# Kernel optimization log

Measured on AMD Instinct MI355X. Metric: run time of the kernel, lower is better.

Reference implementation:

```python
import jax, jax.numpy as jnp
import numpy as np

B, N, F, U, FE, T, E = 2, 50000, 256, 256, 128, 3, 131072


def setup_inputs() -> dict:
    key = jax.random.key(0)
    ks = jax.random.split(key, 7)
    features = jax.random.normal(ks[0], (B, N, F), dtype=jnp.float32)
    edge_idx = jax.random.randint(ks[1], (T, E), 0, B * N, dtype=jnp.int32)  # flattened (b*N+n)
    edge_feats = jax.random.normal(ks[2], (T, E, FE), dtype=jnp.float32)
    W_gate = jax.random.normal(ks[3], (F, U), dtype=jnp.float32) * (1.0 / np.sqrt(F))
    W_gate_e = jax.random.normal(ks[4], (T, FE, U), dtype=jnp.float32) * (1.0 / np.sqrt(FE))
    W_dense = jax.random.normal(ks[5], (T, FE, U), dtype=jnp.float32) * (1.0 / np.sqrt(FE))
    b_dense = jax.random.normal(ks[6], (T, U), dtype=jnp.float32) * 0.01
    return {"features": features, "edge_idx": edge_idx, "edge_feats": edge_feats,
            "W_gate": W_gate, "W_gate_e": W_gate_e, "W_dense": W_dense, "b_dense": b_dense}


def reference(features, edge_idx, edge_feats, W_gate, W_gate_e, W_dense, b_dense):
    b, n, f = features.shape
    u = W_gate.shape[1]
    # shared gate Dense (no bias) applied to all node features; flattened over (B,N)
    src_gated = features.reshape(b * n, f) @ W_gate                      # [B*N, U]
    # per-edge-type gate/value transforms, vectorized over edge types
    gate_e = jnp.einsum('tef,tfu->teu', edge_feats, W_gate_e)            # [T, E, U]
    val_e = jnp.einsum('tef,tfu->teu', edge_feats, W_dense) + b_dense[:, None, :]
    gate = jax.nn.sigmoid(src_gated[edge_idx] + gate_e)                  # gather node gate per edge
    msgs = val_e * gate                                                  # [T, E, U]
    out = jnp.zeros((b * n, u), features.dtype)
    out = out.at[edge_idx.reshape(-1)].add(msgs.reshape(-1, u))          # scatter-add over all edge types
    return out.reshape(b, n, u)
```

## Files before the change

### kernel.cpp

```cpp
#include <hip/hip_runtime.h>
#include <math.h>

#define M1 100000
#define FF 256
#define UU 256
#define FED 128
#define TT 3
#define EE 131072
#define EPB 32
#define TPT 8
#define EPA 32
#define SCAN_B 98

typedef __attribute__((ext_vector_type(8))) short short8;
typedef __attribute__((ext_vector_type(4))) short short4v;
typedef __attribute__((ext_vector_type(4))) float f32x4;

static __device__ __forceinline__ ushort f2bf(float x) {
    union { float f; uint u; } c; c.f = x;
    const uint u = c.u;
    return (ushort)((u + 0x7FFFu + ((u >> 16) & 1u)) >> 16);
}
static __device__ __forceinline__ float bf2f(ushort h) {
    union { uint u; float f; } c; c.u = ((uint)h) << 16;
    return c.f;
}

__global__ __launch_bounds__(256) void k_prep(const float* __restrict__ Wg,
                                              const float* __restrict__ Wge,
                                              const float* __restrict__ Wde,
                                              short* __restrict__ WtG,
                                              short* __restrict__ WtGe,
                                              short* __restrict__ WtDe) {
    const int idx = blockIdx.x * 256 + threadIdx.x;
    if (idx < 65536) {
        const int n = idx >> 8, k = idx & 255;
        WtG[n * 256 + k] = (short)f2bf(Wg[k * 256 + n]);
    } else {
        int j = idx - 65536;
        const float* src = Wge;
        short* dst = WtGe;
        if (j >= 98304) { j -= 98304; src = Wde; dst = WtDe; }
        const int t = j >> 15, rem = j & 32767;
        const int n = rem >> 7, k = rem & 127;
        dst[t * 32768 + n * 128 + k] = (short)f2bf(src[t * 32768 + k * 256 + n]);
    }
}

__global__ __launch_bounds__(256) void k1_srcgate(const float* __restrict__ feats,
                                                  const short* __restrict__ WtG,
                                                  ushort* __restrict__ sg) {
    __shared__ char As[32 * 512];
    const int tid = threadIdx.x, lane = tid & 63, wid = tid >> 6;
    const int r0 = blockIdx.x * 32;

    const float* src = feats + (size_t)r0 * FF;
#pragma unroll
    for (int j = 0; j < 4; ++j) {
        const int chunk = j * 256 + tid;
        const int row = chunk >> 5, kc = chunk & 31;
        const float4 f0 = *(const float4*)(src + row * FF + kc * 8);
        const float4 f1 = *(const float4*)(src + row * FF + kc * 8 + 4);
        short8 v;
        v[0]=(short)f2bf(f0.x); v[1]=(short)f2bf(f0.y); v[2]=(short)f2bf(f0.z); v[3]=(short)f2bf(f0.w);
        v[4]=(short)f2bf(f1.x); v[5]=(short)f2bf(f1.y); v[6]=(short)f2bf(f1.z); v[7]=(short)f2bf(f1.w);
        int byte = row * 512 + kc * 16;
        byte ^= (row & 7) << 4;
        *(short8*)(As + byte) = v;
    }
    __syncthreads();

    const int nb = wid * 64;
    f32x4 acc[2][4];
#pragma unroll
    for (int m = 0; m < 2; ++m)
#pragma unroll
        for (int n = 0; n < 4; ++n) acc[m][n] = (f32x4){0.f, 0.f, 0.f, 0.f};

    for (int ks = 0; ks < 8; ++ks) {
        short8 a[2];
#pragma unroll
        for (int m = 0; m < 2; ++m) {
            const int row = m * 16 + (lane & 15);
            int byte = row * 512 + ks * 64 + (lane >> 4) * 16;
            byte ^= (row & 7) << 4;
            a[m] = *(const short8*)(As + byte);
        }
#pragma unroll
        for (int n = 0; n < 4; ++n) {
            const int col = nb + n * 16 + (lane & 15);
            const short8 b = *(const short8*)(WtG + col * 256 + ks * 32 + (lane >> 4) * 8);
#pragma unroll
            for (int m = 0; m < 2; ++m)
                acc[m][n] = __builtin_amdgcn_mfma_f32_16x16x32_bf16(a[m], b, acc[m][n], 0, 0, 0);
        }
    }
#pragma unroll
    for (int m = 0; m < 2; ++m)
#pragma unroll
        for (int n = 0; n < 4; ++n) {
            const int col = nb + n * 16 + (lane & 15);
#pragma unroll
            for (int r = 0; r < 4; ++r) {
                const int row = m * 16 + (lane >> 4) * 4 + r;
                sg[(size_t)(r0 + row) * UU + col] = f2bf(acc[m][n][r]);
            }
        }
}

__global__ __launch_bounds__(256) void k_hist(const int* __restrict__ eidx,
                                              int* __restrict__ cnt) {
    const int idx = blockIdx.x * 256 + threadIdx.x;
    atomicAdd(&cnt[(idx >> 17) * M1 + eidx[idx]], 1);
}

__global__ __launch_bounds__(1024) void k_scan1(int* __restrict__ cnt,
                                                int* __restrict__ part) {
    const int t = blockIdx.x / SCAN_B, b = blockIdx.x % SCAN_B;
    const int i = b * 1024 + threadIdx.x;
    __shared__ int s[1024];
    const int v = (i < M1) ? cnt[t * M1 + i] : 0;
    s[threadIdx.x] = v;
    __syncthreads();
    for (int off = 1; off < 1024; off <<= 1) {
        const int x = (threadIdx.x >= off) ? s[threadIdx.x - off] : 0;
        __syncthreads();
        s[threadIdx.x] += x;
        __syncthreads();
    }
    if (i < M1) cnt[t * M1 + i] = s[threadIdx.x] - v;
    if (threadIdx.x == 1023) part[blockIdx.x] = s[1023];
}

__global__ void k_scan2(int* __restrict__ part) {
    const int t = threadIdx.x;
    if (t < TT) {
        int run = 0;
        for (int b = 0; b < SCAN_B; ++b) {
            const int p = part[t * SCAN_B + b];
            part[t * SCAN_B + b] = run;
            run += p;
        }
    }
}

__global__ __launch_bounds__(1024) void k_scan3(int* __restrict__ cnt,
                                                const int* __restrict__ part) {
    const int t = blockIdx.x / SCAN_B, b = blockIdx.x % SCAN_B;
    const int i = b * 1024 + threadIdx.x;
    if (i < M1) cnt[t * M1 + i] += part[blockIdx.x];
}

__global__ __launch_bounds__(256) void k_scatter(const int* __restrict__ eidx,
                                                 int* __restrict__ cur,
                                                 int* __restrict__ sorted,
                                                 int* __restrict__ snode) {
    const int idx = blockIdx.x * 256 + threadIdx.x;
    const int t = idx >> 17;
    const int v = eidx[idx];
    const int slot = atomicAdd(&cur[t * M1 + v], 1);
    sorted[t * EE + slot] = idx & (EE - 1);
    snode[t * EE + slot]  = v;
}

__global__ __launch_bounds__(1024, 4) void k2_msgs(const float* __restrict__ efeat,
                                                   const short* __restrict__ WtGe,
                                                   const short* __restrict__ WtDe,
                                                   const float* __restrict__ bd,
                                                   const ushort* __restrict__ sg,
                                                   const int* __restrict__ sorted,
                                                   const int* __restrict__ snode,
                                                   ushort* __restrict__ msgs) {
    __shared__ char As[EPB * 256];
    __shared__ ushort sgl[EPB][264];
    const int tid = threadIdx.x, lane = tid & 63, wid = tid >> 6;
    const int t = blockIdx.y;
    const int tile0 = blockIdx.x * TPT;

    const int col = wid * 16 + (lane & 15);
    const int ksl = (lane >> 4) * 8;
    const short* Bg = WtGe + t * 32768;
    const short* Bd = WtDe + t * 32768;
    short8 wg[4], wv[4];
#pragma unroll
    for (int ks = 0; ks < 4; ++ks) {
        wg[ks] = *(const short8*)(Bg + col * 128 + ks * 32 + ksl);
        wv[ks] = *(const short8*)(Bd + col * 128 + ks * 32 + ksl);
    }
    const float bias = bd[t * UU + col];

    const int erow = tid >> 5, ekc = tid & 31;

    float4 pf_e;
    uint4  pf_g;
    {
        const int base = t * EE + tile0 * EPB;
        const int se = sorted[base + erow];
        pf_e = *(const float4*)(efeat + ((size_t)t * EE + se) * FED + ekc * 4);
        const int nd = snode[base + erow];
        pf_g = *(const uint4*)((const uint*)(sg + (size_t)nd * UU) + ekc * 4);
    }

    for (int it = 0; it < TPT; ++it) {
        const int e0 = (tile0 + it) * EPB;

        {
            short4v v;
            v[0] = (short)f2bf(pf_e.x); v[1] = (short)f2bf(pf_e.y);
            v[2] = (short)f2bf(pf_e.z); v[3] = (short)f2bf(pf_e.w);
            int byte = erow * 256 + ekc * 8;
            byte ^= (erow & 7) << 4;
            *(short4v*)(As + byte) = v;
            *(uint4*)&sgl[erow][ekc * 8] = pf_g;
        }
        __syncthreads();

        if (it + 1 < TPT) {
            const int base = t * EE + (tile0 + it + 1) * EPB;
            const int se = sorted[base + erow];
            pf_e = *(const float4*)(efeat + ((size_t)t * EE + se) * FED + ekc * 4);
            const int nd = snode[base + erow];
            pf_g = *(const uint4*)((const uint*)(sg + (size_t)nd * UU) + ekc * 4);
        }

        f32x4 accg[2], accv[2];
#pragma unroll
        for (int m = 0; m < 2; ++m) {
            accg[m] = (f32x4){0.f, 0.f, 0.f, 0.f};
            accv[m] = (f32x4){bias, bias, bias, bias};
        }
#pragma unroll
        for (int ks = 0; ks < 4; ++ks) {
#pragma unroll
            for (int m = 0; m < 2; ++m) {
                const int row = m * 16 + (lane & 15);
                int byte = row * 256 + ks * 64 + (lane >> 4) * 16;
                byte ^= (row & 7) << 4;
                const short8 a = *(const short8*)(As + byte);
                accg[m] = __builtin_amdgcn_mfma_f32_16x16x32_bf16(a, wg[ks], accg[m], 0, 0, 0);
                accv[m] = __builtin_amdgcn_mfma_f32_16x16x32_bf16(a, wv[ks], accv[m], 0, 0, 0);
            }
        }

#pragma unroll
        for (int m = 0; m < 2; ++m) {
            const int ebase = m * 16 + (lane >> 4) * 4;
#pragma unroll
            for (int r = 0; r < 4; ++r) {
                const float sgv = bf2f(sgl[ebase + r][col]);
                const float e = __expf(-(sgv + accg[m][r]));
                const float g = __builtin_amdgcn_rcpf(1.f + e);
                const float msg = accv[m][r] * g;
                msgs[((size_t)t * EE + e0 + ebase + r) * UU + col] = f2bf(msg);
            }
        }
        __syncthreads();
    }
}

__global__ __launch_bounds__(256, 8) void k3_reduce(const int* __restrict__ cnt,
                                                    const ushort* __restrict__ msgs,
                                                    float* __restrict__ out) {
    const int tid = threadIdx.x, lane = tid & 63, w = tid >> 6;
    const int v = blockIdx.x * 4 + w;
    float a0 = 0.f, a1 = 0.f, a2 = 0.f, a3 = 0.f;
#pragma unroll
    for (int t = 0; t < TT; ++t) {
        const int end   = cnt[t * M1 + v];
        const int start = (v == 0) ? 0 : cnt[t * M1 + v - 1];
        const ushort* base = msgs + (size_t)t * EE * UU + lane * 4;
        int e = start;
        for (; e + 1 < end; e += 2) {
            const uint2 d0 = *(const uint2*)(base + (size_t)e * UU);
            const uint2 d1 = *(const uint2*)(base + (size_t)(e + 1) * UU);
            a0 += bf2f((ushort)(d0.x & 0xffff)) + bf2f((ushort)(d1.x & 0xffff));
            a1 += bf2f((ushort)(d0.x >> 16))    + bf2f((ushort)(d1.x >> 16));
            a2 += bf2f((ushort)(d0.y & 0xffff)) + bf2f((ushort)(d1.y & 0xffff));
            a3 += bf2f((ushort)(d0.y >> 16))    + bf2f((ushort)(d1.y >> 16));
        }
        if (e < end) {
            const uint2 d0 = *(const uint2*)(base + (size_t)e * UU);
            a0 += bf2f((ushort)(d0.x & 0xffff));
            a1 += bf2f((ushort)(d0.x >> 16));
            a2 += bf2f((ushort)(d0.y & 0xffff));
            a3 += bf2f((ushort)(d0.y >> 16));
        }
    }
    float4 o; o.x = a0; o.y = a1; o.z = a2; o.w = a3;
    *(float4*)(out + (size_t)v * UU + lane * 4) = o;
}

__global__ __launch_bounds__(256, 4) void k2_edges(const int* __restrict__ eidx,
                                                   const float* __restrict__ efeat,
                                                   const short* __restrict__ WtGe,
                                                   const short* __restrict__ WtDe,
                                                   const float* __restrict__ bd,
                                                   const ushort* __restrict__ sg,
                                                   const int* __restrict__ sorted,
                                                   float* __restrict__ out) {
    __shared__ char As[EPA * 256];
    __shared__ ushort sgl[EPA][260];
    __shared__ int nds[EPA];
    const int tid = threadIdx.x, lane = tid & 63, wid = tid >> 6;
    const int t = blockIdx.y;
    const int e0 = blockIdx.x * EPA;
    const int* sortedT = sorted + t * EE + e0;
    const int* eidxT   = eidx + t * EE;

    if (tid < EPA) nds[tid] = eidxT[sortedT[tid]];
#pragma unroll
    for (int j = 0; j < 2; ++j) {
        const int chunk = j * 256 + tid;
        const int row = chunk >> 4, kc = chunk & 15;
        const int se = sortedT[row];
        const float* src = efeat + ((size_t)t * EE + se) * FED + kc * 8;
        const float4 f0 = *(const float4*)(src);
        const float4 f1 = *(const float4*)(src + 4);
        short8 v;
        v[0]=(short)f2bf(f0.x); v[1]=(short)f2bf(f0.y); v[2]=(short)f2bf(f0.z); v[3]=(short)f2bf(f0.w);
        v[4]=(short)f2bf(f1.x); v[5]=(short)f2bf(f1.y); v[6]=(short)f2bf(f1.z); v[7]=(short)f2bf(f1.w);
        int byte = row * 256 + kc * 16;
        byte ^= (row & 7) << 4;
        *(short8*)(As + byte) = v;
    }
    __syncthreads();
#pragma unroll
    for (int j = 0; j < 16; ++j) {
        const int item = j * 256 + tid;
        const int row = item >> 7, c2 = item & 127;
        const uint v = *(const uint*)(sg + (size_t)nds[row] * UU + c2 * 2);
        *(uint*)&sgl[row][c2 * 2] = v;
    }
    const short* Bg = WtGe + t * 32768;
    const short* Bd = WtDe + t * 32768;
    const int nb = wid * 64;
    f32x4 accg[2][4], accv[2][4];
#pragma unroll
    for (int m = 0; m < 2; ++m)
#pragma unroll
        for (int n = 0; n < 4; ++n) {
            accg[m][n] = (f32x4){0.f, 0.f, 0.f, 0.f};
            accv[m][n] = (f32x4){0.f, 0.f, 0.f, 0.f};
        }
#pragma unroll
    for (int ks = 0; ks < 4; ++ks) {
        short8 a[2];
#pragma unroll
        for (int m = 0; m < 2; ++m) {
            const int row = m * 16 + (lane & 15);
            int byte = row * 256 + ks * 64 + (lane >> 4) * 16;
            byte ^= (row & 7) << 4;
            a[m] = *(const short8*)(As + byte);
        }
#pragma unroll
        for (int n = 0; n < 4; ++n) {
            const int col = nb + n * 16 + (lane & 15);
            const int koff = ks * 32 + (lane >> 4) * 8;
            const short8 bg = *(const short8*)(Bg + col * 128 + koff);
            const short8 bv = *(const short8*)(Bd + col * 128 + koff);
#pragma unroll
            for (int m = 0; m < 2; ++m) {
                accg[m][n] = __builtin_amdgcn_mfma_f32_16x16x32_bf16(a[m], bg, accg[m][n], 0, 0, 0);
                accv[m][n] = __builtin_amdgcn_mfma_f32_16x16x32_bf16(a[m], bv, accv[m][n], 0, 0, 0);
            }
        }
    }
    __syncthreads();
    float bias[4];
#pragma unroll
    for (int n = 0; n < 4; ++n) bias[n] = bd[t * UU + nb + n * 16 + (lane & 15)];
#pragma unroll
    for (int m = 0; m < 2; ++m) {
        const int ebase = m * 16 + (lane >> 4) * 4;
        int node[4];
#pragma unroll
        for (int r = 0; r < 4; ++r) node[r] = nds[ebase + r];
#pragma unroll
        for (int n = 0; n < 4; ++n) {
            const int col = nb + n * 16 + (lane & 15);
            float carry = 0.f;
#pragma unroll
            for (int r = 0; r < 4; ++r) {
                const float sgv = bf2f(sgl[ebase + r][col]);
                const float e = __expf(-(sgv + accg[m][n][r]));
                const float g = __builtin_amdgcn_rcpf(1.f + e);
                carry += (accv[m][n][r] + bias[n]) * g;
                if (r == 3 || node[r + 1] != node[r]) {
                    atomicAdd(&out[(size_t)node[r] * UU + col], carry);
                    carry = 0.f;
                }
            }
        }
    }
}

extern "C" void kernel_launch(void* const* d_in, const int* in_sizes, int n_in,
                              void* d_out, int out_size, void* d_ws, size_t ws_size,
                              hipStream_t stream) {
    const float* feats = (const float*)d_in[0];
    const int*   eidx  = (const int*)d_in[1];
    const float* efeat = (const float*)d_in[2];
    const float* Wg    = (const float*)d_in[3];
    const float* Wge   = (const float*)d_in[4];
    const float* Wde   = (const float*)d_in[5];
    const float* bd    = (const float*)d_in[6];
    float* out = (float*)d_out;

    char* ws = (char*)d_ws;
    size_t off = 0;
    auto alloc = [&](size_t bytes) { char* p = ws + off; off = (off + bytes + 511) & ~(size_t)511; return p; };
    ushort* sg   = (ushort*)alloc((size_t)M1 * UU * 2);
    short* WtG   = (short*)alloc(256 * 256 * 2);
    short* WtGe  = (short*)alloc((size_t)TT * FED * UU * 2);
    short* WtDe  = (short*)alloc((size_t)TT * FED * UU * 2);
    int* cnt     = (int*)alloc((size_t)TT * M1 * 4);
    int* part    = (int*)alloc(4096);
    int* sorted  = (int*)alloc((size_t)TT * EE * 4);
    int* snode   = (int*)alloc((size_t)TT * EE * 4);
    const size_t small_needed = off;
    ushort* msgs = (ushort*)alloc((size_t)TT * EE * UU * 2);
    const size_t big_needed = off;

    hipMemsetAsync(cnt, 0, (size_t)TT * M1 * 4, stream);
    k_prep<<<262144 / 256, 256, 0, stream>>>(Wg, Wge, Wde, WtG, WtGe, WtDe);
    k1_srcgate<<<M1 / 32, 256, 0, stream>>>(feats, WtG, sg);

    k_hist<<<(TT * EE) / 256, 256, 0, stream>>>(eidx, cnt);
    k_scan1<<<TT * SCAN_B, 1024, 0, stream>>>(cnt, part);
    k_scan2<<<1, 64, 0, stream>>>(part);
    k_scan3<<<TT * SCAN_B, 1024, 0, stream>>>(cnt, part);
    k_scatter<<<(TT * EE) / 256, 256, 0, stream>>>(eidx, cnt, sorted, snode);

    if (ws_size >= big_needed) {
        k2_msgs<<<dim3((EE / EPB) / TPT, TT), 1024, 0, stream>>>(efeat, WtGe, WtDe, bd,
                                                                 (const ushort*)sg, sorted, snode, msgs);
        k3_reduce<<<M1 / 4, 256, 0, stream>>>(cnt, (const ushort*)msgs, out);
    } else if (ws_size >= small_needed) {
        hipMemsetAsync(d_out, 0, (size_t)out_size * sizeof(float), stream);
        k2_edges<<<dim3(EE / EPA, TT), 256, 0, stream>>>(eidx, efeat, WtGe, WtDe, bd,
                                                         (const ushort*)sg, sorted, out);
    }
}
```

Before: 364.4 us.

## Restructure srcgate GEMM with register-resident weights and double-buffered LDS tiles

The source-gate GEMM kernel is rebuilt to use 1024-thread blocks, each handling 5 row tiles. Every wave now keeps its 16-column weight slice in registers, and the next tile's features are prefetched into a double-buffered LDS tile, so the kernel no longer re-reads weights from global memory for each 32-row tile. The message kernel also double-buffers its LDS tiles and drops the trailing barrier. The bf16 conversion is switched to the native __bf16 cast. The risks are extra LDS use that may lower occupancy, and fewer, larger blocks that may fit the machine less evenly.

```diff
diff --git a/kernel.cpp b/kernel.cpp
--- a/kernel.cpp
+++ b/kernel.cpp
@@ -9,6 +9,7 @@
 #define EE 131072
 #define EPB 32
 #define TPT 8
+#define TPT1 5
 #define EPA 32
 #define SCAN_B 98
 
@@ -17,9 +18,7 @@
 typedef __attribute__((ext_vector_type(4))) float f32x4;
 
 static __device__ __forceinline__ ushort f2bf(float x) {
-    union { float f; uint u; } c; c.f = x;
-    const uint u = c.u;
-    return (ushort)((u + 0x7FFFu + ((u >> 16) & 1u)) >> 16);
+    union { __bf16 b; ushort u; } c; c.b = (__bf16)x; return c.u;
 }
 static __device__ __forceinline__ float bf2f(ushort h) {
     union { uint u; float f; } c; c.u = ((uint)h) << 16;
@@ -47,65 +46,71 @@
     }
 }
 
-__global__ __launch_bounds__(256) void k1_srcgate(const float* __restrict__ feats,
-                                                  const short* __restrict__ WtG,
-                                                  ushort* __restrict__ sg) {
-    __shared__ char As[32 * 512];
+__global__ __launch_bounds__(1024, 4) void k1_srcgate(const float* __restrict__ feats,
+                                                      const short* __restrict__ WtG,
+                                                      ushort* __restrict__ sg) {
+    __shared__ char As[2][32 * 512];
     const int tid = threadIdx.x, lane = tid & 63, wid = tid >> 6;
-    const int r0 = blockIdx.x * 32;
-
-    const float* src = feats + (size_t)r0 * FF;
-#pragma unroll
-    for (int j = 0; j < 4; ++j) {
-        const int chunk = j * 256 + tid;
-        const int row = chunk >> 5, kc = chunk & 31;
-        const float4 f0 = *(const float4*)(src + row * FF + kc * 8);
-        const float4 f1 = *(const float4*)(src + row * FF + kc * 8 + 4);
-        short8 v;
-        v[0]=(short)f2bf(f0.x); v[1]=(short)f2bf(f0.y); v[2]=(short)f2bf(f0.z); v[3]=(short)f2bf(f0.w);
-        v[4]=(short)f2bf(f1.x); v[5]=(short)f2bf(f1.y); v[6]=(short)f2bf(f1.z); v[7]=(short)f2bf(f1.w);
-        int byte = row * 512 + kc * 16;
-        byte ^= (row & 7) << 4;
-        *(short8*)(As + byte) = v;
-    }
-    __syncthreads();
-
-    const int nb = wid * 64;
-    f32x4 acc[2][4];
-#pragma unroll
-    for (int m = 0; m < 2; ++m)
-#pragma unroll
-        for (int n = 0; n < 4; ++n) acc[m][n] = (f32x4){0.f, 0.f, 0.f, 0.f};
-
-    for (int ks = 0; ks < 8; ++ks) {
-        short8 a[2];
+    const int tile0 = blockIdx.x * TPT1;
+
+    const int col = wid * 16 + (lane & 15);
+    const int ksl = (lane >> 4) * 8;
+    short8 wb[8];
+#pragma unroll
+    for (int ks = 0; ks < 8; ++ks)
+        wb[ks] = *(const short8*)(WtG + col * 256 + ks * 32 + ksl);
+
+    const int erow = tid >> 5, ekc = tid & 31;
+    float4 pf0, pf1;
+    {
+        const float* src = feats + ((size_t)(tile0 * 32) + erow) * FF + ekc * 8;
+        pf0 = *(const float4*)(src);
+        pf1 = *(const float4*)(src + 4);
+    }
+
+    for (int it = 0; it < TPT1; ++it) {
+        const int p = it & 1;
+        {
+            short8 v;
+            v[0]=(short)f2bf(pf0.x); v[1]=(short)f2bf(pf0.y); v[2]=(short)f2bf(pf0.z); v[3]=(short)f2bf(pf0.w);
+            v[4]=(short)f2bf(pf1.x); v[5]=(short)f2bf(pf1.y); v[6]=(short)f2bf(pf1.z); v[7]=(short)f2bf(pf1.w);
+            int byte = erow * 512 + ekc * 16;
+            byte ^= (erow & 7) << 4;
+            *(short8*)(As[p] + byte) = v;
+        }
+        __syncthreads();
+
+        if (it + 1 < TPT1) {
+            const float* src = feats + ((size_t)((tile0 + it + 1) * 32) + erow) * FF + ekc * 8;
+            pf0 = *(const float4*)(src);
+            pf1 = *(const float4*)(src + 4);
+        }
+
+        f32x4 acc[2];
+#pragma unroll
+        for (int m = 0; m < 2; ++m) acc[m] = (f32x4){0.f, 0.f, 0.f, 0.f};
+#pragma unroll
+        for (int ks = 0; ks < 8; ++ks) {
+#pragma unroll
+            for (int m = 0; m < 2; ++m) {
+                const int row = m * 16 + (lane & 15);
+                int byte = row * 512 + ks * 64 + (lane >> 4) * 16;
+                byte ^= (row & 7) << 4;
+                const short8 a = *(const short8*)(As[p] + byte);
+                acc[m] = __builtin_amdgcn_mfma_f32_16x16x32_bf16(a, wb[ks], acc[m], 0, 0, 0);
+            }
+        }
+
+        const int r0 = (tile0 + it) * 32;
 #pragma unroll
         for (int m = 0; m < 2; ++m) {
-            const int row = m * 16 + (lane & 15);
-            int byte = row * 512 + ks * 64 + (lane >> 4) * 16;
-            byte ^= (row & 7) << 4;
-            a[m] = *(const short8*)(As + byte);
-        }
-#pragma unroll
-        for (int n = 0; n < 4; ++n) {
-            const int col = nb + n * 16 + (lane & 15);
-            const short8 b = *(const short8*)(WtG + col * 256 + ks * 32 + (lane >> 4) * 8);
-#pragma unroll
-            for (int m = 0; m < 2; ++m)
-                acc[m][n] = __builtin_amdgcn_mfma_f32_16x16x32_bf16(a[m], b, acc[m][n], 0, 0, 0);
-        }
-    }
-#pragma unroll
-    for (int m = 0; m < 2; ++m)
-#pragma unroll
-        for (int n = 0; n < 4; ++n) {
-            const int col = nb + n * 16 + (lane & 15);
 #pragma unroll
             for (int r = 0; r < 4; ++r) {
                 const int row = m * 16 + (lane >> 4) * 4 + r;
-                sg[(size_t)(r0 + row) * UU + col] = f2bf(acc[m][n][r]);
-            }
-        }
+                sg[(size_t)(r0 + row) * UU + col] = f2bf(acc[m][r]);
+            }
+        }
+    }
 }
 
 __global__ __launch_bounds__(256) void k_hist(const int* __restrict__ eidx,
@@ -171,8 +176,8 @@
                                                    const int* __restrict__ sorted,
                                                    const int* __restrict__ snode,
                                                    ushort* __restrict__ msgs) {
-    __shared__ char As[EPB * 256];
-    __shared__ ushort sgl[EPB][264];
+    __shared__ char As[2][EPB * 256];
+    __shared__ ushort sgl[2][EPB][264];
     const int tid = threadIdx.x, lane = tid & 63, wid = tid >> 6;
     const int t = blockIdx.y;
     const int tile0 = blockIdx.x * TPT;
@@ -202,6 +207,7 @@
     }
 
     for (int it = 0; it < TPT; ++it) {
+        const int p = it & 1;
         const int e0 = (tile0 + it) * EPB;
 
         {
@@ -210,8 +216,8 @@
             v[2] = (short)f2bf(pf_e.z); v[3] = (short)f2bf(pf_e.w);
             int byte = erow * 256 + ekc * 8;
             byte ^= (erow & 7) << 4;
-            *(short4v*)(As + byte) = v;
-            *(uint4*)&sgl[erow][ekc * 8] = pf_g;
+            *(short4v*)(As[p] + byte) = v;
+            *(uint4*)&sgl[p][erow][ekc * 8] = pf_g;
         }
         __syncthreads();
 
@@ -236,7 +242,7 @@
                 const int row = m * 16 + (lane & 15);
                 int byte = row * 256 + ks * 64 + (lane >> 4) * 16;
                 byte ^= (row & 7) << 4;
-                const short8 a = *(const short8*)(As + byte);
+                const short8 a = *(const short8*)(As[p] + byte);
                 accg[m] = __builtin_amdgcn_mfma_f32_16x16x32_bf16(a, wg[ks], accg[m], 0, 0, 0);
                 accv[m] = __builtin_amdgcn_mfma_f32_16x16x32_bf16(a, wv[ks], accv[m], 0, 0, 0);
             }
@@ -247,14 +253,13 @@
             const int ebase = m * 16 + (lane >> 4) * 4;
 #pragma unroll
             for (int r = 0; r < 4; ++r) {
-                const float sgv = bf2f(sgl[ebase + r][col]);
+                const float sgv = bf2f(sgl[p][ebase + r][col]);
                 const float e = __expf(-(sgv + accg[m][r]));
                 const float g = __builtin_amdgcn_rcpf(1.f + e);
                 const float msg = accv[m][r] * g;
                 msgs[((size_t)t * EE + e0 + ebase + r) * UU + col] = f2bf(msg);
             }
         }
-        __syncthreads();
     }
 }
 
@@ -423,7 +428,7 @@
 
     hipMemsetAsync(cnt, 0, (size_t)TT * M1 * 4, stream);
     k_prep<<<262144 / 256, 256, 0, stream>>>(Wg, Wge, Wde, WtG, WtGe, WtDe);
-    k1_srcgate<<<M1 / 32, 256, 0, stream>>>(feats, WtG, sg);
+    k1_srcgate<<<M1 / 32 / TPT1, 1024, 0, stream>>>(feats, WtG, sg);
 
     k_hist<<<(TT * EE) / 256, 256, 0, stream>>>(eidx, cnt);
     k_scan1<<<TT * SCAN_B, 1024, 0, stream>>>(cnt, part);
```

Result: faster. 344.0 us (-5.6%).
